# Performance work log

Hardware: AMD Instinct MI355X
Metric: run time of the kernel (lower is better)

The kernel has to match this reference:

```python
import jax, jax.numpy as jnp
import numpy as np

DIM, HEADS, HEAD_DIM = 1024, 16, 64
B, S = 2, 1024
LAMBDA = 4.0
EPS = 1e-6


def setup_inputs() -> dict:
    key = jax.random.key(0)
    ks = jax.random.split(key, 7)
    sc = 1.0 / np.sqrt(DIM)
    return {
        "x": jax.random.normal(ks[0], (B, S, DIM), jnp.float32),
        "qkv_w": jax.random.normal(ks[1], (3 * DIM, DIM), jnp.float32) * sc,
        "qkv_b": jax.random.normal(ks[2], (3 * DIM,), jnp.float32) * 0.01,
        "proj_w": jax.random.normal(ks[3], (DIM, DIM), jnp.float32) * sc,
        "proj_b": jax.random.normal(ks[4], (DIM,), jnp.float32) * 0.01,
        "dwc_w": jax.random.normal(ks[5], (DIM, 1, 3), jnp.float32) * 0.3,
        "dwc_b": jax.random.normal(ks[6], (DIM,), jnp.float32) * 0.01,
    }


def _l1_dist(q, k):
    # q,k: [B,H,S,Dh] -> pairwise L1 distance [B,H,S,S].
    # Accumulate over head_dim with a (rematerialized) scan so we never
    # materialize the [B,H,S,S,Dh] broadcast tensor.
    qT = jnp.moveaxis(q, -1, 0)  # [Dh,B,H,S]
    kT = jnp.moveaxis(k, -1, 0)

    def step(acc, qk):
        qd, kd = qk  # [B,H,S]
        return acc + jnp.abs(qd[..., :, None] - kd[..., None, :]), None

    init = jnp.zeros(q.shape[:-1] + (k.shape[-2],), q.dtype)
    dist, _ = jax.lax.scan(jax.checkpoint(step), init, (qT, kT))
    return dist


def reference(x, qkv_w, qkv_b, proj_w, proj_b, dwc_w, dwc_b):
    Bq, Sq, C = x.shape
    # qkv projection -> q,k,v each [B,H,S,Dh]
    qkv = (x @ qkv_w.T + qkv_b).reshape(Bq, Sq, 3, HEADS, HEAD_DIM)
    qkv = jnp.transpose(qkv, (2, 0, 3, 1, 4))
    q, k, v = qkv[0], qkv[1], qkv[2]

    # exact Laplacian (L1-distance) kernel attention, row-normalized
    dist = _l1_dist(q, k)                       # [B,H,S,S]
    kern = jnp.exp(-LAMBDA * dist / HEAD_DIM)   # mean-L1 scaling
    attn = kern / (jnp.sum(kern, axis=-1, keepdims=True) + EPS)
    global_attn = jnp.einsum("bhij,bhjd->bhid", attn, v)

    # depthwise conv1d local branch on v (channel order = head-major)
    v1d = jnp.transpose(v, (0, 1, 3, 2)).reshape(Bq, C, Sq)  # [B,C,S]
    local = jax.lax.conv_general_dilated(
        v1d, dwc_w, window_strides=(1,), padding=((1, 1),),
        feature_group_count=C, dimension_numbers=("NCH", "OIH", "NCH"))
    local = local + dwc_b[None, :, None]
    local = jnp.transpose(local.reshape(Bq, HEADS, HEAD_DIM, Sq), (0, 1, 3, 2))

    y = global_attn + local                      # [B,H,S,Dh]
    y = jnp.transpose(y, (0, 2, 1, 3)).reshape(Bq, Sq, C)
    return y @ proj_w.T + proj_b
```

## Files before the change

kernel.cpp:

```cpp
#include <hip/hip_runtime.h>

#define DIMC 1024
#define HEADS 16
#define HD 64
#define BATCH 2
#define SEQ 1024
#define NQKV 3072

typedef _Float16 f16;
typedef _Float16 half8 __attribute__((ext_vector_type(8)));
typedef _Float16 half4v __attribute__((ext_vector_type(4)));
typedef float floatx4 __attribute__((ext_vector_type(4)));

__device__ __forceinline__ void gld16(const void* g, void* l) {
  __builtin_amdgcn_global_load_lds((const __attribute__((address_space(1))) void*)g,
                                   (__attribute__((address_space(3))) void*)l, 16, 0, 0);
}

__device__ __forceinline__ unsigned sadU8(unsigned a, unsigned b, unsigned c) {
#if __has_builtin(__builtin_amdgcn_sad_u8)
  return __builtin_amdgcn_sad_u8(a, b, c);
#else
  unsigned d;
  asm("v_sad_u8 %0, %1, %2, %3" : "=v"(d) : "v"(a), "v"(b), "v"(c));
  return d;
#endif
}

__global__ __launch_bounds__(256) void cvt_kernel(
    const float* __restrict__ x, const float* __restrict__ wq, const float* __restrict__ wp,
    f16* __restrict__ x16, f16* __restrict__ wq16, f16* __restrict__ wp16)
{
  long long bid = blockIdx.x;
  const float* src; f16* dst; long long base;
  if (bid < 2048)            { src = x;  dst = x16;  base = bid; }
  else if (bid < 2048+3072)  { src = wq; dst = wq16; base = bid - 2048; }
  else                       { src = wp; dst = wp16; base = bid - (2048+3072); }
  long long i = base*256 + threadIdx.x;
  float4 v = ((const float4*)src)[i];
  half4v h; h[0]=(f16)v.x; h[1]=(f16)v.y; h[2]=(f16)v.z; h[3]=(f16)v.w;
  *(half4v*)(dst + i*4) = h;
}

template<int TM, int TN, int BK, int MODE>
__global__ __launch_bounds__(256, 3) void gemm_kernel(
    const f16* __restrict__ A, const f16* __restrict__ Bw, const float* __restrict__ bias,
    unsigned char* __restrict__ q8, unsigned char* __restrict__ k8, f16* __restrict__ vT,
    float* __restrict__ outp, int K)
{
  constexpr int MT = TM / 32;
  constexpr int NT = TN / 32;
  constexpr int G  = BK / 8;
  __shared__ f16 As[TM*BK];
  __shared__ f16 Bs[TN*BK];
  const int tid = threadIdx.x;
  const int wave = tid >> 6, lane = tid & 63;
  const int lq = lane >> 4, li = lane & 15;
  const int m0 = blockIdx.y * TM, n0 = blockIdx.x * TN;
  const int wm = (wave & 1) * (TM/2), wn = (wave >> 1) * (TN/2);
  floatx4 acc[MT][NT] = {};

  const int kIters = K / BK;
  for (int kt = 0; kt < kIters; ++kt) {
    __syncthreads();
#pragma unroll
    for (int r = 0; r < TM*BK/2048; ++r) {
      int slot = r*256 + tid;
      int row = slot / G, c = slot % G, g = c ^ (row & (G-1));
      gld16(A + (size_t)(m0+row)*K + kt*BK + g*8, As + slot*8);
    }
#pragma unroll
    for (int r = 0; r < TN*BK/2048; ++r) {
      int slot = r*256 + tid;
      int row = slot / G, c = slot % G, g = c ^ (row & (G-1));
      gld16(Bw + (size_t)(n0+row)*K + kt*BK + g*8, Bs + slot*8);
    }
    __syncthreads();
#pragma unroll
    for (int ks = 0; ks < BK/32; ++ks) {
      half8 af[MT], bf[NT];
      int kc = ks*4 + lq;
#pragma unroll
      for (int t = 0; t < MT; ++t) {
        int am = wm + t*16 + li;
        af[t] = *(const half8*)&As[am*BK + (kc ^ (am & (G-1)))*8];
      }
#pragma unroll
      for (int t = 0; t < NT; ++t) {
        int bn = wn + t*16 + li;
        bf[t] = *(const half8*)&Bs[bn*BK + (kc ^ (bn & (G-1)))*8];
      }
#pragma unroll
      for (int mt = 0; mt < MT; ++mt)
#pragma unroll
        for (int nt = 0; nt < NT; ++nt)
          acc[mt][nt] = __builtin_amdgcn_mfma_f32_16x16x32_f16(af[mt], bf[nt], acc[mt][nt], 0, 0, 0);
    }
  }

#pragma unroll
  for (int mt = 0; mt < MT; ++mt) {
#pragma unroll
    for (int nt = 0; nt < NT; ++nt) {
      int f = n0 + wn + nt*16 + li;
      float bb = bias[f];
      if (MODE == 0) {
        int which = f >> 10, cc = f & 1023, h = cc >> 6, d = cc & 63;
        int t0 = m0 + wm + mt*16 + lq*4;
        int b = t0 >> 10, s0 = t0 & 1023;
        if (which == 2) {
          half4v hv;
#pragma unroll
          for (int r = 0; r < 4; ++r) hv[r] = (f16)(acc[mt][nt][r] + bb);
          *(half4v*)&vT[((size_t)((b*HEADS + h)*HD + d))*SEQ + s0] = hv;
        } else {
          unsigned char* dst = (which == 0) ? q8 : k8;
#pragma unroll
          for (int r = 0; r < 4; ++r) {
            float v = acc[mt][nt][r] + bb;
            int u = (int)floorf(v * 16.0f + 128.5f);
            u = u < 0 ? 0 : (u > 255 ? 255 : u);
            dst[((size_t)((b*HEADS + h)*SEQ + s0 + r))*HD + d] = (unsigned char)u;
          }
        }
      } else {
#pragma unroll
        for (int r = 0; r < 4; ++r) {
          int t = m0 + wm + mt*16 + lq*4 + r;
          outp[(size_t)t*DIMC + f] = acc[mt][nt][r] + bb;
        }
      }
    }
  }
}

__global__ __launch_bounds__(256, 3) void attn_kernel(
    const unsigned char* __restrict__ q8g, const unsigned char* __restrict__ k8g,
    const f16* __restrict__ vTg, const float* __restrict__ dwcw, const float* __restrict__ dwcb,
    f16* __restrict__ y16)
{
  __shared__ unsigned char q8s[32*64];
  __shared__ unsigned char k8s[2][128*64];
  __shared__ f16 sfrag[2][8*64*8];
  __shared__ float rspart[32*4];
  __shared__ float rowsumS[32];
  __shared__ f16 vconv[64*34];

  const int tid = threadIdx.x;
  const int bh = blockIdx.y;
  const int i0 = blockIdx.x * 32;
  const int lane = tid & 63, wave = tid >> 6;
  const int lq = lane >> 4, li = lane & 15;
  const int iL = tid & 7;
  const int jt = tid >> 3;
  const int sub = (jt >> 1) & 3, par = jt & 1;
  const int mtb = wave & 1, ntb = wave >> 1;

  if (wave < 2)
    gld16(q8g + ((size_t)bh*SEQ + i0)*HD + tid*16, q8s + tid*16);

  {
    int d = tid >> 2, part = tid & 3;
    const f16* vrow = vTg + ((size_t)(bh*HD) + d)*SEQ;
#pragma unroll
    for (int e = 0; e < 9; ++e) {
      int ss = part*9 + e;
      if (ss < 34) {
        int s = i0 - 1 + ss;
        vconv[d*34 + ss] = (s >= 0 && s < SEQ) ? vrow[s] : (f16)0.0f;
      }
    }
  }

  auto stageK = [&](int buf, int jb) {
    const unsigned char* kg = k8g + ((size_t)bh*SEQ + jb*128)*HD;
#pragma unroll
    for (int r = 0; r < 2; ++r) {
      int slot = r*256 + tid;
      int row = slot >> 2, g = (slot & 3) ^ ((row >> 2) & 3);
      gld16(kg + row*64 + g*16, k8s[buf] + slot*16);
    }
  };

  stageK(0, 0);
  __syncthreads();

  unsigned qr[4][16];
#pragma unroll
  for (int n = 0; n < 4; ++n)
#pragma unroll
    for (int c4 = 0; c4 < 4; ++c4) {
      uint4 t = *(const uint4*)&q8s[(iL + 8*n)*64 + c4*16];
      qr[n][c4*4+0] = t.x; qr[n][c4*4+1] = t.y; qr[n][c4*4+2] = t.z; qr[n][c4*4+3] = t.w;
    }

  float rs[4] = {0.f, 0.f, 0.f, 0.f};
  floatx4 pacc[2] = {};

  for (int jb = 0; jb < 8; ++jb) {
    const int cur = jb & 1;
    const int j0 = jb * 128;

    if (jb < 7) stageK(cur ^ 1, jb + 1);

    half8 bfr[2][4];
#pragma unroll
    for (int nt = 0; nt < 2; ++nt)
#pragma unroll
      for (int ks = 0; ks < 4; ++ks)
        bfr[nt][ks] = *(const half8*)(vTg + ((size_t)(bh*HD) + (ntb*2+nt)*16 + li)*SEQ
                                      + j0 + ks*32 + lq*8);

    const unsigned char* kb = k8s[cur];

    unsigned sacc[4][4] = {};
#pragma unroll
    for (int c4 = 0; c4 < 4; ++c4) {
      uint4 kk[4];
#pragma unroll
      for (int jj = 0; jj < 4; ++jj)
        kk[jj] = *(const uint4*)&kb[(jt*4 + jj)*64 + (c4 ^ (jt & 3))*16];
#pragma unroll
      for (int n = 0; n < 4; ++n)
#pragma unroll
        for (int jj = 0; jj < 4; ++jj) {
          sacc[n][jj] = sadU8(qr[n][c4*4+0], kk[jj].x, sacc[n][jj]);
          sacc[n][jj] = sadU8(qr[n][c4*4+1], kk[jj].y, sacc[n][jj]);
          sacc[n][jj] = sadU8(qr[n][c4*4+2], kk[jj].z, sacc[n][jj]);
          sacc[n][jj] = sadU8(qr[n][c4*4+3], kk[jj].w, sacc[n][jj]);
        }
    }

#pragma unroll
    for (int n = 0; n < 4; ++n) {
      half4v sv;
#pragma unroll
      for (int jj = 0; jj < 4; ++jj) {
        float sf = exp2f(-0.0056355275f * (float)sacc[n][jj]);
        rs[n] += sf;
        sv[jj] = (f16)sf;
      }
      int frow = iL + 8*(n & 1);
      *(half4v*)&sfrag[cur][(((n>>1)*4 + wave)*64 + sub*16 + (frow ^ (sub*2)))*8 + par*4] = sv;
    }

    __syncthreads();

#pragma unroll
    for (int ks = 0; ks < 4; ++ks) {
      half8 a = *(const half8*)&sfrag[cur][((mtb*4 + ks)*64 + lq*16 + (li ^ (lq*2)))*8];
#pragma unroll
      for (int nt = 0; nt < 2; ++nt)
        pacc[nt] = __builtin_amdgcn_mfma_f32_16x16x32_f16(a, bfr[nt][ks], pacc[nt], 0, 0, 0);
    }
  }

#pragma unroll
  for (int n = 0; n < 4; ++n) {
    rs[n] += __shfl_xor(rs[n], 8, 64);
    rs[n] += __shfl_xor(rs[n], 16, 64);
    rs[n] += __shfl_xor(rs[n], 32, 64);
  }
  if (lane < 8) {
#pragma unroll
    for (int n = 0; n < 4; ++n) rspart[(iL + 8*n)*4 + wave] = rs[n];
  }
  __syncthreads();
  if (tid < 32)
    rowsumS[tid] = rspart[tid*4+0] + rspart[tid*4+1] + rspart[tid*4+2] + rspart[tid*4+3] + 1e-6f;
  __syncthreads();

  const int b = bh >> 4, h = bh & 15;
#pragma unroll
  for (int nt = 0; nt < 2; ++nt) {
    int d = (ntb*2 + nt)*16 + li;
    int c = h*64 + d;
    float w0 = dwcw[c*3+0], w1 = dwcw[c*3+1], w2 = dwcw[c*3+2], cb = dwcb[c];
#pragma unroll
    for (int r = 0; r < 4; ++r) {
      int ii = mtb*16 + lq*4 + r;
      float val = pacc[nt][r] / rowsumS[ii];
      val += w0*(float)vconv[d*34 + ii] + w1*(float)vconv[d*34 + ii + 1]
           + w2*(float)vconv[d*34 + ii + 2] + cb;
      int s = i0 + ii;
      y16[((size_t)(b*SEQ + s))*DIMC + c] = (f16)val;
    }
  }
}

extern "C" void kernel_launch(void* const* d_in, const int* in_sizes, int n_in,
                              void* d_out, int out_size, void* d_ws, size_t ws_size,
                              hipStream_t stream) {
  const float* x      = (const float*)d_in[0];
  const float* qkv_w  = (const float*)d_in[1];
  const float* qkv_b  = (const float*)d_in[2];
  const float* proj_w = (const float*)d_in[3];
  const float* proj_b = (const float*)d_in[4];
  const float* dwc_w  = (const float*)d_in[5];
  const float* dwc_b  = (const float*)d_in[6];
  float* out = (float*)d_out;

  char* ws = (char*)d_ws;
  f16* x16  = (f16*)(ws);
  f16* wq16 = (f16*)(ws + (4ll<<20));
  f16* wp16 = (f16*)(ws + (10ll<<20));
  unsigned char* q8 = (unsigned char*)(ws + (12ll<<20));
  unsigned char* k8 = (unsigned char*)(ws + (14ll<<20));
  f16* vT   = (f16*)(ws + (16ll<<20));
  f16* y16  = (f16*)(ws + (20ll<<20));

  cvt_kernel<<<6144, 256, 0, stream>>>(x, qkv_w, proj_w, x16, wq16, wp16);
  gemm_kernel<64,128,128,0><<<dim3(24, 32), 256, 0, stream>>>(x16, wq16, qkv_b, q8, k8, vT, nullptr, DIMC);
  attn_kernel<<<dim3(32, 32), 256, 0, stream>>>(q8, k8, vT, dwc_w, dwc_b, y16);
  gemm_kernel<64,64,128,1><<<dim3(16, 32), 256, 0, stream>>>(y16, wp16, proj_b, nullptr, nullptr, nullptr, out, DIMC);
}
```

Baseline: 168.1 us.

## Split key range across waves with per-wave SAD/MFMA and LDS atomic reduction

Restructures the attention kernel so each wave owns a disjoint quarter of the keys and loops over them independently. K is read straight from global memory into registers with double-buffered prefetch instead of being staged through shared memory, so the per-iteration block barrier goes away. Each wave computes partial P·V for all 32 rows and 64 dims, and the partials and row sums are then merged through LDS float atomics. Each wave now holds more accumulator registers, so launch bounds drop to 2 blocks per SM, and the epilogue writes vectorized half8 stores.

```diff
diff --git a/kernel.cpp b/kernel.cpp
--- a/kernel.cpp
+++ b/kernel.cpp
@@ -134,15 +134,26 @@
   }
 }
 
-__global__ __launch_bounds__(256, 3) void attn_kernel(
+#define SAD_BLOCK(C4, KK) \
+  _Pragma("unroll") \
+  for (int n = 0; n < 4; ++n) { \
+    _Pragma("unroll") \
+    for (int jj = 0; jj < 4; ++jj) { \
+      sacc[n][jj] = sadU8(qr[n][(C4)*4+0], KK[jj].x, sacc[n][jj]); \
+      sacc[n][jj] = sadU8(qr[n][(C4)*4+1], KK[jj].y, sacc[n][jj]); \
+      sacc[n][jj] = sadU8(qr[n][(C4)*4+2], KK[jj].z, sacc[n][jj]); \
+      sacc[n][jj] = sadU8(qr[n][(C4)*4+3], KK[jj].w, sacc[n][jj]); \
+    } \
+  }
+
+__global__ __launch_bounds__(256, 2) void attn_kernel(
     const unsigned char* __restrict__ q8g, const unsigned char* __restrict__ k8g,
     const f16* __restrict__ vTg, const float* __restrict__ dwcw, const float* __restrict__ dwcb,
     f16* __restrict__ y16)
 {
   __shared__ unsigned char q8s[32*64];
-  __shared__ unsigned char k8s[2][128*64];
-  __shared__ f16 sfrag[2][8*64*8];
-  __shared__ float rspart[32*4];
+  __shared__ f16 sfragW[4*2*64*8];
+  __shared__ float Obuf[32*64];
   __shared__ float rowsumS[32];
   __shared__ f16 vconv[64*34];
 
@@ -151,10 +162,12 @@
   const int i0 = blockIdx.x * 32;
   const int lane = tid & 63, wave = tid >> 6;
   const int lq = lane >> 4, li = lane & 15;
-  const int iL = tid & 7;
-  const int jt = tid >> 3;
-  const int sub = (jt >> 1) & 3, par = jt & 1;
-  const int mtb = wave & 1, ntb = wave >> 1;
+  const int iL = lane & 7;
+  const int jt = lane >> 3;
+
+#pragma unroll
+  for (int i = 0; i < 8; ++i) Obuf[tid + i*256] = 0.0f;
+  if (tid < 32) rowsumS[tid] = 1e-6f;
 
   if (wave < 2)
     gld16(q8g + ((size_t)bh*SEQ + i0)*HD + tid*16, q8s + tid*16);
@@ -171,18 +184,6 @@
       }
     }
   }
-
-  auto stageK = [&](int buf, int jb) {
-    const unsigned char* kg = k8g + ((size_t)bh*SEQ + jb*128)*HD;
-#pragma unroll
-    for (int r = 0; r < 2; ++r) {
-      int slot = r*256 + tid;
-      int row = slot >> 2, g = (slot & 3) ^ ((row >> 2) & 3);
-      gld16(kg + row*64 + g*16, k8s[buf] + slot*16);
-    }
-  };
-
-  stageK(0, 0);
   __syncthreads();
 
   unsigned qr[4][16];
@@ -194,42 +195,38 @@
       qr[n][c4*4+0] = t.x; qr[n][c4*4+1] = t.y; qr[n][c4*4+2] = t.z; qr[n][c4*4+3] = t.w;
     }
 
+  const unsigned char* kptr = k8g + ((size_t)bh*SEQ + wave*256)*HD + jt*256;
+  const f16* vbase = vTg + (size_t)(bh*HD)*SEQ + wave*256 + lq*8;
+
+  uint4 kkA[4], kkB[4];
+#pragma unroll
+  for (int jj = 0; jj < 4; ++jj) kkA[jj] = *(const uint4*)(kptr + jj*64);
+
   float rs[4] = {0.f, 0.f, 0.f, 0.f};
-  floatx4 pacc[2] = {};
-
-  for (int jb = 0; jb < 8; ++jb) {
-    const int cur = jb & 1;
-    const int j0 = jb * 128;
-
-    if (jb < 7) stageK(cur ^ 1, jb + 1);
-
-    half8 bfr[2][4];
-#pragma unroll
-    for (int nt = 0; nt < 2; ++nt)
-#pragma unroll
-      for (int ks = 0; ks < 4; ++ks)
-        bfr[nt][ks] = *(const half8*)(vTg + ((size_t)(bh*HD) + (ntb*2+nt)*16 + li)*SEQ
-                                      + j0 + ks*32 + lq*8);
-
-    const unsigned char* kb = k8s[cur];
+  floatx4 pacc[2][4] = {};
+
+  for (int c = 0; c < 8; ++c) {
+    half8 bfr[4];
+#pragma unroll
+    for (int dt = 0; dt < 4; ++dt)
+      bfr[dt] = *(const half8*)(vbase + (size_t)(dt*16 + li)*SEQ + c*32);
 
     unsigned sacc[4][4] = {};
 #pragma unroll
-    for (int c4 = 0; c4 < 4; ++c4) {
-      uint4 kk[4];
-#pragma unroll
-      for (int jj = 0; jj < 4; ++jj)
-        kk[jj] = *(const uint4*)&kb[(jt*4 + jj)*64 + (c4 ^ (jt & 3))*16];
-#pragma unroll
-      for (int n = 0; n < 4; ++n)
-#pragma unroll
-        for (int jj = 0; jj < 4; ++jj) {
-          sacc[n][jj] = sadU8(qr[n][c4*4+0], kk[jj].x, sacc[n][jj]);
-          sacc[n][jj] = sadU8(qr[n][c4*4+1], kk[jj].y, sacc[n][jj]);
-          sacc[n][jj] = sadU8(qr[n][c4*4+2], kk[jj].z, sacc[n][jj]);
-          sacc[n][jj] = sadU8(qr[n][c4*4+3], kk[jj].w, sacc[n][jj]);
-        }
-    }
+    for (int jj = 0; jj < 4; ++jj) kkB[jj] = *(const uint4*)(kptr + jj*64 + 16);
+    SAD_BLOCK(0, kkA)
+#pragma unroll
+    for (int jj = 0; jj < 4; ++jj) kkA[jj] = *(const uint4*)(kptr + jj*64 + 32);
+    SAD_BLOCK(1, kkB)
+#pragma unroll
+    for (int jj = 0; jj < 4; ++jj) kkB[jj] = *(const uint4*)(kptr + jj*64 + 48);
+    SAD_BLOCK(2, kkA)
+    if (c < 7) {
+#pragma unroll
+      for (int jj = 0; jj < 4; ++jj) kkA[jj] = *(const uint4*)(kptr + 2048 + jj*64);
+    }
+    SAD_BLOCK(3, kkB)
+    kptr += 2048;
 
 #pragma unroll
     for (int n = 0; n < 4; ++n) {
@@ -240,18 +237,15 @@
         rs[n] += sf;
         sv[jj] = (f16)sf;
       }
-      int frow = iL + 8*(n & 1);
-      *(half4v*)&sfrag[cur][(((n>>1)*4 + wave)*64 + sub*16 + (frow ^ (sub*2)))*8 + par*4] = sv;
-    }
-
-    __syncthreads();
-
-#pragma unroll
-    for (int ks = 0; ks < 4; ++ks) {
-      half8 a = *(const half8*)&sfrag[cur][((mtb*4 + ks)*64 + lq*16 + (li ^ (lq*2)))*8];
-#pragma unroll
-      for (int nt = 0; nt < 2; ++nt)
-        pacc[nt] = __builtin_amdgcn_mfma_f32_16x16x32_f16(a, bfr[nt][ks], pacc[nt], 0, 0, 0);
+      *(half4v*)&sfragW[(((wave*2 + (n>>1))*64) + (iL + 8*(n&1)) + 16*(jt>>1))*8 + (jt&1)*4] = sv;
+    }
+
+#pragma unroll
+    for (int t = 0; t < 2; ++t) {
+      half8 a = *(const half8*)&sfragW[((wave*2 + t)*64 + lane)*8];
+#pragma unroll
+      for (int dt = 0; dt < 4; ++dt)
+        pacc[t][dt] = __builtin_amdgcn_mfma_f32_16x16x32_f16(a, bfr[dt], pacc[t][dt], 0, 0, 0);
     }
   }
 
@@ -263,29 +257,33 @@
   }
   if (lane < 8) {
 #pragma unroll
-    for (int n = 0; n < 4; ++n) rspart[(iL + 8*n)*4 + wave] = rs[n];
-  }
+    for (int n = 0; n < 4; ++n) atomicAdd(&rowsumS[iL + 8*n], rs[n]);
+  }
+#pragma unroll
+  for (int t = 0; t < 2; ++t)
+#pragma unroll
+    for (int dt = 0; dt < 4; ++dt)
+#pragma unroll
+      for (int r = 0; r < 4; ++r)
+        atomicAdd(&Obuf[(t*16 + lq*4 + r)*64 + dt*16 + li], pacc[t][dt][r]);
   __syncthreads();
-  if (tid < 32)
-    rowsumS[tid] = rspart[tid*4+0] + rspart[tid*4+1] + rspart[tid*4+2] + rspart[tid*4+3] + 1e-6f;
-  __syncthreads();
 
   const int b = bh >> 4, h = bh & 15;
-#pragma unroll
-  for (int nt = 0; nt < 2; ++nt) {
-    int d = (ntb*2 + nt)*16 + li;
-    int c = h*64 + d;
-    float w0 = dwcw[c*3+0], w1 = dwcw[c*3+1], w2 = dwcw[c*3+2], cb = dwcb[c];
-#pragma unroll
-    for (int r = 0; r < 4; ++r) {
-      int ii = mtb*16 + lq*4 + r;
-      float val = pacc[nt][r] / rowsumS[ii];
-      val += w0*(float)vconv[d*34 + ii] + w1*(float)vconv[d*34 + ii + 1]
-           + w2*(float)vconv[d*34 + ii + 2] + cb;
-      int s = i0 + ii;
-      y16[((size_t)(b*SEQ + s))*DIMC + c] = (f16)val;
-    }
-  }
+  const int r = tid >> 3, p = tid & 7;
+  float inv = 1.0f / rowsumS[r];
+  half8 hv;
+#pragma unroll
+  for (int e = 0; e < 8; ++e) {
+    int d = p*8 + e;
+    int cch = h*64 + d;
+    float val = Obuf[r*64 + d] * inv
+              + dwcw[cch*3+0] * (float)vconv[d*34 + r]
+              + dwcw[cch*3+1] * (float)vconv[d*34 + r + 1]
+              + dwcw[cch*3+2] * (float)vconv[d*34 + r + 2]
+              + dwcb[cch];
+    hv[e] = (f16)val;
+  }
+  *(half8*)(y16 + ((size_t)(b*SEQ + i0 + r))*DIMC + h*64 + p*8) = hv;
 }
 
 extern "C" void kernel_launch(void* const* d_in, const int* in_sizes, int n_in,
```

New measurement: 190.7 us. 1.13x slower.
